# Kernel optimization log

Measured on AMD Instinct MI355X. Metric: run time of the kernel, lower is better.

## Reference

```python
import jax, jax.numpy as jnp
import numpy as np

NEG = -1e30  # safe -inf surrogate (avoids nan grads through where)
NUM_CLASSES = 128
BLANK = NUM_CLASSES - 1
B, T, L = 256, 512, 64


def setup_inputs() -> dict:
    key = jax.random.key(0)
    k1, k2, k3, k4 = jax.random.split(key, 4)
    y_pred = jax.random.normal(k1, (B, T, NUM_CLASSES), dtype=jnp.float32)
    y_true = jax.random.randint(k2, (B, L), 0, BLANK, dtype=jnp.int32)  # labels in [0, C-2]
    input_length = jax.random.randint(k3, (B,), T // 2, T + 1, dtype=jnp.int32)
    label_length = jax.random.randint(k4, (B,), L // 2, L + 1, dtype=jnp.int32)
    return {"y_true": y_true, "y_pred": y_pred,
            "input_length": input_length, "label_length": label_length}


def ctc_loss(y_pred, y_true, input_length, label_length):
    # y_pred: [B,T,C] logits (batch-major), y_true: [B,L] int labels, blank = C-1.
    Bs, Ts, C = y_pred.shape
    Ls = y_true.shape[1]
    S = 2 * Ls + 1  # extended label lattice: blank, l1, blank, l2, ..., blank
    lp = jax.nn.log_softmax(y_pred.astype(jnp.float32), axis=-1)  # [B,T,C]
    z = jnp.full((Bs, S), BLANK, dtype=jnp.int32).at[:, 1::2].set(y_true)  # [B,S]
    idx = jnp.broadcast_to(z[:, None, :], (Bs, Ts, S))
    lp_z = jnp.take_along_axis(lp, idx, axis=2)  # [B,T,S] log p(z_s | t)
    # skip transition s-2 -> s allowed when z_s is a label differing from z_{s-2}
    s_idx = jnp.arange(S)
    z_m2 = jnp.pad(z[:, :-2], ((0, 0), (2, 0)), constant_values=BLANK)
    skip = (s_idx[None, :] >= 2) & (z != BLANK) & (z != z_m2)  # [B,S]
    alpha0 = (jnp.full((Bs, S), NEG, jnp.float32)
              .at[:, 0].set(lp_z[:, 0, 0])
              .at[:, 1].set(lp_z[:, 0, 1]))
    lps = jnp.moveaxis(lp_z[:, 1:, :], 1, 0)  # [T-1, B, S]
    ts = jnp.arange(1, Ts)

    def step(alpha, xs):
        t, lpt = xs
        a1 = jnp.pad(alpha[:, :-1], ((0, 0), (1, 0)), constant_values=NEG)
        a2 = jnp.where(skip, jnp.pad(alpha[:, :-2], ((0, 0), (2, 0)), constant_values=NEG), NEG)
        new = jnp.logaddexp(jnp.logaddexp(alpha, a1), a2) + lpt
        # freeze rows whose sequence already ended (t >= input_length)
        alpha = jnp.where((t < input_length)[:, None], new, alpha)
        return alpha, None

    alphaT, _ = jax.lax.scan(step, alpha0, (ts, lps))
    e1 = (2 * label_length)[:, None]  # final blank position per row
    a_end = jnp.take_along_axis(alphaT, e1, axis=1)[:, 0]
    a_end2 = jnp.take_along_axis(alphaT, e1 - 1, axis=1)[:, 0]
    return -jnp.logaddexp(a_end, a_end2)  # [B] negative log-likelihood


def reference(y_true, y_pred, input_length, label_length):
    # tf.nn.ctc_loss(labels, logits, label_length, logit_length,
    #                logits_time_major=False, blank_index=num_classes-1)
    return ctc_loss(y_pred, y_true, input_length, label_length)
```

## Files before the change

kernel.cpp:

```cpp
#include <hip/hip_runtime.h>
#include <hip/hip_fp16.h>
#include <math.h>


constexpr int Cc = 128;
constexpr int Tt = 512;
constexpr int Ll = 64;
constexpr int NPS = 7;
constexpr float INV_LN2 = 1.4426950408889634f;
constexpr float LN2_F   = 0.6931471805599453f;
constexpr float RENORM_THR = 16777216.0f;

__device__ __forceinline__ float fexp2(float x) { return __builtin_amdgcn_exp2f(x); }
__device__ __forceinline__ float flog2(float x) { return __builtin_amdgcn_logf(x); }

template<int CTRL, bool BC>
__device__ __forceinline__ float dppf(float old, float x) {
    return __int_as_float(__builtin_amdgcn_update_dpp(
        __float_as_int(old), __float_as_int(x), CTRL, 0xF, 0xF, BC));
}
__device__ __forceinline__ float wshr1(float x, float fill) { return dppf<0x138, false>(fill, x); }
__device__ __forceinline__ float wshl1(float x, float fill) { return dppf<0x130, false>(fill, x); }

__device__ __forceinline__ float rowsum(float e) {
    e += dppf<0x111, true>(0.f, e);
    e += dppf<0x112, true>(0.f, e);
    e += dppf<0x114, true>(0.f, e);
    e += dppf<0x118, true>(0.f, e);
    return e;
}
__device__ __forceinline__ float xmax64(float m) {
    m = fmaxf(m, __shfl_xor(m, 32, 64));
    m = fmaxf(m, __shfl_xor(m, 16, 64));
    m = fmaxf(m, __shfl_xor(m,  8, 64));
    m = fmaxf(m, __shfl_xor(m,  4, 64));
    m = fmaxf(m, __shfl_xor(m,  2, 64));
    m = fmaxf(m, __shfl_xor(m,  1, 64));
    return m;
}
__device__ __forceinline__ float sflf(float v, int lane) { return __shfl(v, lane, 64); }

__device__ __forceinline__ float bperm_f(int srclane, float v) {
    return __int_as_float(__builtin_amdgcn_ds_bpermute(srclane << 2, __float_as_int(v)));
}
__device__ __forceinline__ float gather4(float4 v, int srclane, int csel) {
    const float gx = bperm_f(srclane, v.x), gy = bperm_f(srclane, v.y);
    const float gz = bperm_f(srclane, v.z), gw = bperm_f(srclane, v.w);
    const float lo = (csel & 1) ? gy : gx;
    const float hi = (csel & 1) ? gw : gz;
    return (csel & 2) ? hi : lo;
}
__device__ __forceinline__ double shflx_d(double v, int mask) {
    const long long x = __double_as_longlong(v);
    int lo = (int)(x & 0xffffffffLL), hi = (int)(x >> 32);
    lo = __shfl_xor(lo, mask, 64);
    hi = __shfl_xor(hi, mask, 64);
    return __longlong_as_double(((long long)hi << 32) | (unsigned)(unsigned int)lo);
}

__device__ __forceinline__ void unpack8(uint4 raw, float (&dv)[8]) {
    const __half2 h0 = *reinterpret_cast<const __half2*>(&raw.x);
    const __half2 h1 = *reinterpret_cast<const __half2*>(&raw.y);
    const __half2 h2 = *reinterpret_cast<const __half2*>(&raw.z);
    const __half2 h3 = *reinterpret_cast<const __half2*>(&raw.w);
    dv[0] = __low2float(h0); dv[1] = __high2float(h0);
    dv[2] = __low2float(h1); dv[3] = __high2float(h1);
    dv[4] = __low2float(h2); dv[5] = __high2float(h2);
    dv[6] = __low2float(h3); dv[7] = __high2float(h3);
}

template<bool GUARD>
__device__ __forceinline__ void do_chunk(uint4 raw, int t0, int inlen, float skf,
                                         float& aO, float& aE, float& r0, float& Rtot)
{
    float dv[8]; unpack8(raw, dv);
    float sd[8];
#pragma unroll
    for (int j = 0; j < 8; ++j) sd[j] = skf * dv[j];
#pragma unroll
    for (int j = 0; j < 8; ++j) {
        if (!GUARD || (t0 + j < inlen)) {
            const float ad = aO * dv[j];
            const float pE = wshr1(aE, r0);
            const float pO = wshr1(aO, 0.0f);
            const float nO = fmaf(pE, dv[j], fmaf(pO, sd[j], ad));
            aE += aO;
            aO = nO;
        }
    }
    const float mx = fmaxf(fmaxf(aO, aE), r0);
    if (__any(mx >= RENORM_THR)) {
        const float M_ = xmax64(mx);
        int R_ = (int)(__float_as_uint(M_) >> 23) - 127;
        R_ = (R_ < 0) ? 0 : ((R_ > 126) ? 126 : R_);
        const float sc = __uint_as_float((unsigned)(127 - R_) << 23);
        aO = fminf(aO * sc, 4.0f);
        aE = fminf(aE * sc, 4.0f);
        r0 = fminf(r0 * sc, 4.0f);
        Rtot += (float)R_;
    }
}

template<bool GUARD>
__device__ __forceinline__ void do_chunk_bwd(uint4 raw, int t0, int inlen, float skfb,
                                             float& bO, float& bE, float& br, float& Rb,
                                             int l)
{
    float dv[8]; unpack8(raw, dv);
#pragma unroll
    for (int j = 7; j >= 0; --j) {
        if (!GUARD || (t0 + j < inlen)) {
            const float BOw = bO * dv[j];
            const float uO  = wshl1(BOw, 0.0f);
            const float t1  = bE + BOw;
            bE += uO;
            br += BOw;
            bO  = fmaf(skfb, uO, t1);
        }
    }
    const float brm = (l == 0) ? br : 0.0f;
    const float mx = fmaxf(fmaxf(bO, bE), brm);
    if (__any(mx >= RENORM_THR)) {
        const float M_ = xmax64(mx);
        int R_ = (int)(__float_as_uint(M_) >> 23) - 127;
        R_ = (R_ < 0) ? 0 : ((R_ > 126) ? 126 : R_);
        const float sc = __uint_as_float((unsigned)(127 - R_) << 23);
        bO = bO * sc;
        bE = bE * sc;
        br = br * sc;
        Rb += (float)R_;
    }
}

__global__ __launch_bounds__(1024, 1) void ctc_fused8_kernel(
    const int* __restrict__ y_true,
    const float* __restrict__ y_pred,
    const int* __restrict__ in_len,
    const int* __restrict__ lab_len,
    float* __restrict__ out)
{
    __shared__ __half w_lds[Tt / 8][64][8];
    __shared__ float  ps[2 * NPS];
    __shared__ int    fctr[5], bctr[5];
    __shared__ int    bdone, pdone;
    __shared__ float  bstate[130];

    const int b   = blockIdx.x;
    const int tid = threadIdx.x;
    const int w   = tid >> 6;
    const int l   = tid & 63;

    if (tid < 5) { fctr[tid] = 0; bctr[tid] = 0; }
    if (tid == 0) { bdone = 0; pdone = 0; }
    __syncthreads();

    int inlen = in_len[b]; if (inlen < 1) inlen = 1; if (inlen > Tt) inlen = Tt;
    int LLv   = lab_len[b]; if (LLv < 1) LLv = 1; if (LLv > Ll) LLv = Ll;

    const int nct  = (inlen + 7) >> 3;
    const int nchf = nct >> 1;
    const int nchb = nct - nchf;

    const int lab = y_true[b * Ll + l] & 127;
    const float* rowbase = y_pred + (size_t)b * Tt * Cc;

    if (w >= 2) {
        const bool asc = (w < 9);
        const int pw    = asc ? (w - 2) : (w - 9);
        const int nside = asc ? nchf : nchb;
        const int half = l >> 5, li = l & 31;
        const int srcA = lab >> 2;
        const int csel = lab & 3;
        const bool live = (l < LLv);
        int* ctr = asc ? fctr : bctr;

        float acc = 0.0f;

        if (pw < nside) {
            const int c0 = asc ? pw : (nct - 1 - pw);
            float4 vb[4];
#pragma unroll
            for (int j = 0; j < 4; ++j)
                vb[j] = ((const float4*)(rowbase + (size_t)(c0 * 8 + 2 * j + half) * Cc))[li];

            for (int k = pw, idx = 0; k < nside; k += NPS, ++idx) {
                const int c  = asc ? k : (nct - 1 - k);
                const int kn = k + NPS;
                const int cn = (kn < nside) ? (asc ? kn : (nct - 1 - kn)) : 0;
                float prod = 1.0f, bsum = 0.0f;
#pragma unroll
                for (int j = 0; j < 4; ++j) {
                    const float4 v = vb[j];
                    vb[j] = ((const float4*)(rowbase + (size_t)(cn * 8 + 2 * j + half) * Cc))[li];

                    const int rA = c * 8 + 2 * j;
                    const int rB = rA + 1;

                    float e = (fexp2(v.x * INV_LN2) + fexp2(v.y * INV_LN2))
                            + (fexp2(v.z * INV_LN2) + fexp2(v.w * INV_LN2));
                    e = rowsum(e);
                    const float sA = sflf(e, 15) + sflf(e, 31);
                    const float sB = sflf(e, 47) + sflf(e, 63);
                    const float blA = sflf(v.w, 31);
                    const float blB = sflf(v.w, 63);

                    const bool okA = rA < inlen, okB = rB < inlen;
                    prod *= okB ? sA * sB : (okA ? sA : 1.0f);
                    bsum += okB ? blA + blB : (okA ? blA : 0.0f);

                    const float xA = gather4(v, srcA, csel);
                    const float xB = gather4(v, srcA + 32, csel);
                    float wA = fminf(fmaxf(fexp2((xA - blA) * INV_LN2), 6.1e-5f), 8192.0f);
                    float wB = fminf(fmaxf(fexp2((xB - blB) * INV_LN2), 6.1e-5f), 8192.0f);
                    wA = live ? wA : 0.0f;
                    wB = live ? wB : 0.0f;
                    const unsigned packed =
                          (unsigned)__half_as_ushort(__float2half(wA))
                        | ((unsigned)__half_as_ushort(__float2half(wB)) << 16);
                    *(unsigned*)&w_lds[c][l][2 * j] = packed;
                }
                acc = fmaf(bsum, INV_LN2, acc) - flog2(prod);
                asm volatile("s_waitcnt lgkmcnt(0)" ::: "memory");
                if (l == 0) atomicAdd(&ctr[idx], 1);
            }
        }
        if (l == 0) ps[(asc ? 0 : NPS) + pw] = acc;
        asm volatile("s_waitcnt lgkmcnt(0)" ::: "memory");
        if (l == 0) atomicAdd(&pdone, 1);
        return;
    }

    const int labp = __shfl_up(lab, 1, 64);
    const float skf = ((l >= 1) && (lab != labp)) ? 1.0f : 0.0f;

    if (w == 1) {
        const float skfb = __shfl(skf, (l + 1) & 63, 64);
        float bE = (l == LLv - 1) ? 1.0f : 0.0f;
        float bO = bE;
        float br = 0.0f, Rb = 0.0f;

        volatile int* vd = bctr;
        int readyd = 0, rrd = 0;
        auto wait_d = [&](int cb) {
            const int needcnt = nct - cb;
            while (readyd < needcnt) {
                const int rem  = nchb - rrd * NPS;
                const int need = rem < NPS ? rem : NPS;
                if (vd[rrd] >= need) { readyd += need; ++rrd; }
                else __builtin_amdgcn_s_sleep(1);
            }
            asm volatile("" ::: "memory");
        };

        if (nchb > 0) {
            wait_d(nct - 1);
            uint4 A = *(const uint4*)&w_lds[nct - 1][l][0];
            for (int cb = nct - 1; cb >= nchf; --cb) {
                uint4 Bv = A;
                if (cb - 1 >= nchf) { wait_d(cb - 1); Bv = *(const uint4*)&w_lds[cb - 1][l][0]; }
                const int t0 = cb * 8;
                if (t0 + 8 <= inlen) do_chunk_bwd<false>(A, t0, inlen, skfb, bO, bE, br, Rb, l);
                else                 do_chunk_bwd<true >(A, t0, inlen, skfb, bO, bE, br, Rb, l);
                A = Bv;
            }
        }
        bstate[l]      = bE;
        bstate[64 + l] = bO;
        if (l == 0) { bstate[128] = br; bstate[129] = Rb; }
        asm volatile("s_waitcnt lgkmcnt(0)" ::: "memory");
        if (l == 0) atomicExch(&bdone, 1);
        return;
    }

    float aO = 0.0f, aE = 0.0f, r0 = 1.0f, Rf = 0.0f;

    volatile int* vf = fctr;
    int readyf = 0, rrf = 0;
    auto wait_f = [&](int cneed) {
        while (readyf <= cneed) {
            const int rem  = nchf - rrf * NPS;
            const int need = rem < NPS ? rem : NPS;
            if (vf[rrf] >= need) { readyf += need; ++rrf; }
            else __builtin_amdgcn_s_sleep(1);
        }
        asm volatile("" ::: "memory");
    };

    if (nchf > 0) {
        wait_f(0);
        uint4 A = *(const uint4*)&w_lds[0][l][0];
        for (int c = 0; c < nchf; ++c) {
            uint4 Bv = A;
            if (c + 1 < nchf) { wait_f(c + 1); Bv = *(const uint4*)&w_lds[c + 1][l][0]; }
            const int t0 = c * 8;
            if (t0 + 8 <= inlen) do_chunk<false>(A, t0, inlen, skf, aO, aE, r0, Rf);
            else                 do_chunk<true >(A, t0, inlen, skf, aO, aE, r0, Rf);
            A = Bv;
        }
    }

    {
        volatile int* vp = &pdone;
        while (*vp < 2 * NPS) __builtin_amdgcn_s_sleep(1);
        volatile int* vbd = &bdone;
        while (*vbd == 0) __builtin_amdgcn_s_sleep(1);
        asm volatile("" ::: "memory");
    }

    float cum_b = 0.0f;
#pragma unroll
    for (int q = 0; q < 2 * NPS; ++q) cum_b += ps[q];

    const float bEl = bstate[l], bOl = bstate[64 + l];
    const float br0 = bstate[128], Rb = bstate[129];
    double cd = (double)aE * (double)bEl + (double)aO * (double)bOl;
    if (l == 0) cd += (double)r0 * (double)br0;
#pragma unroll
    for (int mk = 1; mk < 64; mk <<= 1) cd += shflx_d(cd, mk);
    double sd_ = cd > 1e-300 ? cd : 1e-300;
    const long long u = __double_as_longlong(sd_);
    const int e2 = (int)((u >> 52) & 0x7ff) - 1023;
    const double mant = __longlong_as_double((u & 0xfffffffffffffLL) | 0x3ff0000000000000LL);
    const float l2s = (float)e2 + flog2((float)mant);
    if (l == 0)
        out[b] = -LN2_F * (l2s + Rf + Rb + cum_b);
}

extern "C" void kernel_launch(void* const* d_in, const int* in_sizes, int n_in,
                              void* d_out, int out_size, void* d_ws, size_t ws_size,
                              hipStream_t stream) {
    const int*   y_true  = (const int*)d_in[0];
    const float* y_pred  = (const float*)d_in[1];
    const int*   in_len  = (const int*)d_in[2];
    const int*   lab_len = (const int*)d_in[3];
    float*       out     = (float*)d_out;
    (void)d_ws; (void)ws_size;

    ctc_fused8_kernel<<<256, 1024, 0, stream>>>(y_true, y_pred, in_len, lab_len, out);
}
```

Before: 109.0 us.

## Switch producer warps to one-row-per-wave float2 layout with readlane reductions

The producer warps now load each time row as float2 per lane across the whole wave, rather than splitting two rows across half-waves as float4. Row sums and the blank logit are broadcast with scalar readlane instead of shuffles, and the label gather needs 2 bpermutes per row instead of 4. Each chunk writes its 8 half weights with a single 16-byte LDS store. The cross-chunk register prefetch is gone, so load latency is now exposed per chunk, and there are twice as many exp and rowsum passes per row. The counter arrays are enlarged to 10.

```diff
diff --git a/kernel.cpp b/kernel.cpp
--- a/kernel.cpp
+++ b/kernel.cpp
@@ -22,6 +22,9 @@
 __device__ __forceinline__ float wshr1(float x, float fill) { return dppf<0x138, false>(fill, x); }
 __device__ __forceinline__ float wshl1(float x, float fill) { return dppf<0x130, false>(fill, x); }
 
+__device__ __forceinline__ float rlf(float v, int lane) {
+    return __int_as_float(__builtin_amdgcn_readlane(__float_as_int(v), lane));
+}
 __device__ __forceinline__ float rowsum(float e) {
     e += dppf<0x111, true>(0.f, e);
     e += dppf<0x112, true>(0.f, e);
@@ -38,17 +41,8 @@
     m = fmaxf(m, __shfl_xor(m,  1, 64));
     return m;
 }
-__device__ __forceinline__ float sflf(float v, int lane) { return __shfl(v, lane, 64); }
-
 __device__ __forceinline__ float bperm_f(int srclane, float v) {
     return __int_as_float(__builtin_amdgcn_ds_bpermute(srclane << 2, __float_as_int(v)));
-}
-__device__ __forceinline__ float gather4(float4 v, int srclane, int csel) {
-    const float gx = bperm_f(srclane, v.x), gy = bperm_f(srclane, v.y);
-    const float gz = bperm_f(srclane, v.z), gw = bperm_f(srclane, v.w);
-    const float lo = (csel & 1) ? gy : gx;
-    const float hi = (csel & 1) ? gw : gz;
-    return (csel & 2) ? hi : lo;
 }
 __device__ __forceinline__ double shflx_d(double v, int mask) {
     const long long x = __double_as_longlong(v);
@@ -132,7 +126,7 @@
     }
 }
 
-__global__ __launch_bounds__(1024, 1) void ctc_fused8_kernel(
+__global__ __launch_bounds__(1024, 1) void ctc_fused9_kernel(
     const int* __restrict__ y_true,
     const float* __restrict__ y_pred,
     const int* __restrict__ in_len,
@@ -141,7 +135,7 @@
 {
     __shared__ __half w_lds[Tt / 8][64][8];
     __shared__ float  ps[2 * NPS];
-    __shared__ int    fctr[5], bctr[5];
+    __shared__ int    fctr[10], bctr[10];
     __shared__ int    bdone, pdone;
     __shared__ float  bstate[130];
 
@@ -150,7 +144,7 @@
     const int w   = tid >> 6;
     const int l   = tid & 63;
 
-    if (tid < 5) { fctr[tid] = 0; bctr[tid] = 0; }
+    if (tid < 10) { fctr[tid] = 0; bctr[tid] = 0; }
     if (tid == 0) { bdone = 0; pdone = 0; }
     __syncthreads();
 
@@ -168,61 +162,49 @@
         const bool asc = (w < 9);
         const int pw    = asc ? (w - 2) : (w - 9);
         const int nside = asc ? nchf : nchb;
-        const int half = l >> 5, li = l & 31;
-        const int srcA = lab >> 2;
-        const int csel = lab & 3;
+        const int glane = lab >> 1;
+        const int lsel  = lab & 1;
         const bool live = (l < LLv);
         int* ctr = asc ? fctr : bctr;
 
         float acc = 0.0f;
 
-        if (pw < nside) {
-            const int c0 = asc ? pw : (nct - 1 - pw);
-            float4 vb[4];
-#pragma unroll
-            for (int j = 0; j < 4; ++j)
-                vb[j] = ((const float4*)(rowbase + (size_t)(c0 * 8 + 2 * j + half) * Cc))[li];
-
-            for (int k = pw, idx = 0; k < nside; k += NPS, ++idx) {
-                const int c  = asc ? k : (nct - 1 - k);
-                const int kn = k + NPS;
-                const int cn = (kn < nside) ? (asc ? kn : (nct - 1 - kn)) : 0;
-                float prod = 1.0f, bsum = 0.0f;
-#pragma unroll
-                for (int j = 0; j < 4; ++j) {
-                    const float4 v = vb[j];
-                    vb[j] = ((const float4*)(rowbase + (size_t)(cn * 8 + 2 * j + half) * Cc))[li];
-
-                    const int rA = c * 8 + 2 * j;
-                    const int rB = rA + 1;
-
-                    float e = (fexp2(v.x * INV_LN2) + fexp2(v.y * INV_LN2))
-                            + (fexp2(v.z * INV_LN2) + fexp2(v.w * INV_LN2));
-                    e = rowsum(e);
-                    const float sA = sflf(e, 15) + sflf(e, 31);
-                    const float sB = sflf(e, 47) + sflf(e, 63);
-                    const float blA = sflf(v.w, 31);
-                    const float blB = sflf(v.w, 63);
-
-                    const bool okA = rA < inlen, okB = rB < inlen;
-                    prod *= okB ? sA * sB : (okA ? sA : 1.0f);
-                    bsum += okB ? blA + blB : (okA ? blA : 0.0f);
-
-                    const float xA = gather4(v, srcA, csel);
-                    const float xB = gather4(v, srcA + 32, csel);
-                    float wA = fminf(fmaxf(fexp2((xA - blA) * INV_LN2), 6.1e-5f), 8192.0f);
-                    float wB = fminf(fmaxf(fexp2((xB - blB) * INV_LN2), 6.1e-5f), 8192.0f);
-                    wA = live ? wA : 0.0f;
-                    wB = live ? wB : 0.0f;
-                    const unsigned packed =
-                          (unsigned)__half_as_ushort(__float2half(wA))
-                        | ((unsigned)__half_as_ushort(__float2half(wB)) << 16);
-                    *(unsigned*)&w_lds[c][l][2 * j] = packed;
-                }
-                acc = fmaf(bsum, INV_LN2, acc) - flog2(prod);
-                asm volatile("s_waitcnt lgkmcnt(0)" ::: "memory");
-                if (l == 0) atomicAdd(&ctr[idx], 1);
-            }
+        for (int k = pw, idx = 0; k < nside; k += NPS, ++idx) {
+            const int c = asc ? k : (nct - 1 - k);
+            const int row0 = c * 8;
+            float2 rv[8];
+#pragma unroll
+            for (int t = 0; t < 8; ++t)
+                rv[t] = ((const float2*)(rowbase + (size_t)(row0 + t) * Cc))[l];
+
+            float prod = 1.0f, bsum = 0.0f;
+            uint4 pk;
+
+            auto wbits = [&](int t) -> unsigned {
+                const float2 v = rv[t];
+                float e = fexp2(v.x * INV_LN2) + fexp2(v.y * INV_LN2);
+                e = rowsum(e);
+                const float s  = (rlf(e, 15) + rlf(e, 31)) + (rlf(e, 47) + rlf(e, 63));
+                const float bl = rlf(v.y, 63);
+                const bool ok = (row0 + t) < inlen;
+                prod *= ok ? s : 1.0f;
+                bsum += ok ? bl : 0.0f;
+                const float xa = bperm_f(glane, v.x);
+                const float xb = bperm_f(glane, v.y);
+                const float xl = lsel ? xb : xa;
+                float ww = fminf(fmaxf(fexp2((xl - bl) * INV_LN2), 6.1e-5f), 8192.0f);
+                ww = live ? ww : 0.0f;
+                return (unsigned)__half_as_ushort(__float2half(ww));
+            };
+            pk.x = wbits(0) | (wbits(1) << 16);
+            pk.y = wbits(2) | (wbits(3) << 16);
+            pk.z = wbits(4) | (wbits(5) << 16);
+            pk.w = wbits(6) | (wbits(7) << 16);
+
+            acc = fmaf(bsum, INV_LN2, acc) - flog2(prod);
+            *(uint4*)&w_lds[c][l][0] = pk;
+            asm volatile("s_waitcnt lgkmcnt(0)" ::: "memory");
+            if (l == 0) atomicAdd(&ctr[idx], 1);
         }
         if (l == 0) ps[(asc ? 0 : NPS) + pw] = acc;
         asm volatile("s_waitcnt lgkmcnt(0)" ::: "memory");
@@ -336,5 +318,5 @@
     float*       out     = (float*)d_out;
     (void)d_ws; (void)ws_size;
 
-    ctc_fused8_kernel<<<256, 1024, 0, stream>>>(y_true, y_pred, in_len, lab_len, out);
-}
+    ctc_fused9_kernel<<<256, 1024, 0, stream>>>(y_true, y_pred, in_len, lab_len, out);
+}
```

After: 108.6 us. About the same (-0.3%).
